# Kernel optimization log

Hardware: AMD Instinct MI355X
Metric: run time of the kernel (lower is better)

The kernel has to match this reference:

```python
import jax, jax.numpy as jnp
import numpy as np

DIM = 1024
H = 16
DH = 64
ORDER = 3
TOPK = 64
SCALE = DH ** (-0.5)


def setup_inputs() -> dict:
    key = jax.random.key(0)
    k0, k1, k2 = jax.random.split(key, 3)
    B, N = 2, 2048
    inner = H * DH
    x = jax.random.normal(k0, (B, N, DIM), jnp.float32)
    Wqkv = jax.random.normal(k1, (DIM, 3 * inner), jnp.float32) * (DIM ** -0.5)
    bqkv = jnp.zeros((3 * inner,), jnp.float32)
    Wout = jax.random.normal(k2, (inner, DIM), jnp.float32) * (inner ** -0.5)
    bout = jnp.zeros((DIM,), jnp.float32)
    # init_as_standard_attention for sigmoid act: zero_val=-5, one_val=+5 on row 1
    alphas_raw = jnp.full((ORDER + 1, H), -5.0, jnp.float32).at[1].set(5.0)
    return {"x": x, "Wqkv": Wqkv, "bqkv": bqkv, "Wout": Wout, "bout": bout,
            "alphas_raw": alphas_raw}


def reference(x, Wqkv, bqkv, Wout, bout, alphas_raw):
    B, N, _ = x.shape
    qkv = x @ Wqkv + bqkv                          # [B,N,3*inner]
    q, k, v = jnp.split(qkv, 3, axis=-1)
    to_heads = lambda t: t.reshape(B, N, H, DH).transpose(0, 2, 1, 3)  # [B,H,N,DH]
    q, k, v = to_heads(q), to_heads(k), to_heads(v)
    scores = jnp.einsum('bhnd,bhmd->bhnm', q, k) * SCALE
    # top-k sparsification: drop entries strictly below the k-th largest per row
    if TOPK and TOPK < N:
        kth = jax.lax.top_k(scores, TOPK)[0][..., -1:]  # [B,H,N,1]
        scores = jnp.where(scores < kth, -jnp.inf, scores)
    attn = jax.nn.softmax(scores, axis=-1)          # [B,H,N,N]
    # polynomial graph filter in fp32 (monomial basis, learn_zero_order=False)
    alphas = jax.nn.sigmoid(alphas_raw)             # [ORDER+1, H]
    v_curr = v
    res = jnp.zeros_like(v)
    for i in range(1, ORDER + 1):
        v_curr = jnp.einsum('bhnm,bhmd->bhnd', attn, v_curr)
        res = res + alphas[i][None, :, None, None] * v_curr
    out = res.transpose(0, 2, 1, 3).reshape(B, N, H * DH)
    return out @ Wout + bout
```

## Files before the change

kernel.cpp:

```cpp
#include <hip/hip_runtime.h>
#include <cstdint>
#include <cstddef>

#define HHEADS 16
#define DHEAD  64
#define NSEQ   2048
#define NBATCH 2
#define NDIM   1024
#define TOPKN  64
#define CAP    68
#define NROWS  (NBATCH*HHEADS*NSEQ)

__global__ __launch_bounds__(256) void qkv_gemm(
    const float* __restrict__ x, const float* __restrict__ W,
    const float* __restrict__ bias,
    float* __restrict__ qout, float* __restrict__ kout, float* __restrict__ vout)
{
    __shared__ float As[16][128];
    __shared__ float Bs[16][128];
    const int tid = threadIdx.x;
    const int rowBase = blockIdx.y * 128;
    const int colBase = blockIdx.x * 128;
    const int tx = tid & 15, ty = tid >> 4;
    const int arow = tid & 127, akq = tid >> 7;
    const int bkk = tid >> 5,  bc4 = tid & 31;

    float acc[8][8] = {};
    float4 a0 = *reinterpret_cast<const float4*>(&x[(size_t)(rowBase + arow) * NDIM + akq * 4]);
    float4 a1 = *reinterpret_cast<const float4*>(&x[(size_t)(rowBase + arow) * NDIM + (akq + 2) * 4]);
    float4 b0 = *reinterpret_cast<const float4*>(&W[(size_t)bkk * 3072 + colBase + bc4 * 4]);
    float4 b1 = *reinterpret_cast<const float4*>(&W[(size_t)(bkk + 8) * 3072 + colBase + bc4 * 4]);

    for (int k0 = 0; k0 < NDIM; k0 += 16) {
        __syncthreads();
        As[akq * 4 + 0][arow] = a0.x; As[akq * 4 + 1][arow] = a0.y;
        As[akq * 4 + 2][arow] = a0.z; As[akq * 4 + 3][arow] = a0.w;
        As[(akq + 2) * 4 + 0][arow] = a1.x; As[(akq + 2) * 4 + 1][arow] = a1.y;
        As[(akq + 2) * 4 + 2][arow] = a1.z; As[(akq + 2) * 4 + 3][arow] = a1.w;
        *reinterpret_cast<float4*>(&Bs[bkk][bc4 * 4])     = b0;
        *reinterpret_cast<float4*>(&Bs[bkk + 8][bc4 * 4]) = b1;
        __syncthreads();
        if (k0 + 16 < NDIM) {
            a0 = *reinterpret_cast<const float4*>(&x[(size_t)(rowBase + arow) * NDIM + k0 + 16 + akq * 4]);
            a1 = *reinterpret_cast<const float4*>(&x[(size_t)(rowBase + arow) * NDIM + k0 + 16 + (akq + 2) * 4]);
            b0 = *reinterpret_cast<const float4*>(&W[(size_t)(k0 + 16 + bkk) * 3072 + colBase + bc4 * 4]);
            b1 = *reinterpret_cast<const float4*>(&W[(size_t)(k0 + 16 + bkk + 8) * 3072 + colBase + bc4 * 4]);
        }
#pragma unroll
        for (int kk = 0; kk < 16; kk++) {
            float4 alo = *reinterpret_cast<const float4*>(&As[kk][ty * 4]);
            float4 ahi = *reinterpret_cast<const float4*>(&As[kk][64 + ty * 4]);
            float4 blo = *reinterpret_cast<const float4*>(&Bs[kk][tx * 4]);
            float4 bhi = *reinterpret_cast<const float4*>(&Bs[kk][64 + tx * 4]);
            float ar[8] = {alo.x, alo.y, alo.z, alo.w, ahi.x, ahi.y, ahi.z, ahi.w};
            float br[8] = {blo.x, blo.y, blo.z, blo.w, bhi.x, bhi.y, bhi.z, bhi.w};
#pragma unroll
            for (int i = 0; i < 8; i++)
#pragma unroll
                for (int j = 0; j < 8; j++) acc[i][j] += ar[i] * br[j];
        }
    }

    const int which = colBase >> 10;
    float* dst = which == 0 ? qout : (which == 1 ? kout : vout);
#pragma unroll
    for (int jh = 0; jh < 2; jh++) {
        const int colh = colBase + jh * 64 + tx * 4;
        const int h = (colh & 1023) >> 6;
        const int d0 = colh & 63;
        float4 bb = *reinterpret_cast<const float4*>(&bias[colh]);
#pragma unroll
        for (int ih = 0; ih < 2; ih++)
#pragma unroll
            for (int i = 0; i < 4; i++) {
                int r = rowBase + ih * 64 + ty * 4 + i;
                int b = r >> 11, n = r & 2047;
                size_t o = ((size_t)((b << 4) + h) * NSEQ + n) * DHEAD + d0;
                float4 st;
                st.x = acc[ih * 4 + i][jh * 4 + 0] + bb.x;
                st.y = acc[ih * 4 + i][jh * 4 + 1] + bb.y;
                st.z = acc[ih * 4 + i][jh * 4 + 2] + bb.z;
                st.w = acc[ih * 4 + i][jh * 4 + 3] + bb.w;
                *reinterpret_cast<float4*>(&dst[o]) = st;
            }
    }
}

__device__ __forceinline__ uint32_t f2key(float f) {
    uint32_t u = __float_as_uint(f);
    return (u & 0x80000000u) ? ~u : (u | 0x80000000u);
}
__device__ __forceinline__ float key2f(uint32_t k) {
    uint32_t u = (k & 0x80000000u) ? (k & 0x7FFFFFFFu) : ~k;
    return __uint_as_float(u);
}

__device__ __forceinline__ void topk_emit(
    uint32_t (&k)[32], float m, int row, int lane,
    int* __restrict__ tki, float* __restrict__ tkp, int* __restrict__ tkc)
{
    uint32_t lo = 0u, hi = 0xFFFFFFFFu;
    while (lo < hi) {
        uint32_t mid = (uint32_t)(((uint64_t)lo + (uint64_t)hi + 1ull) >> 1);
        int c = 0;
#pragma unroll
        for (int t = 0; t < 32; t++)
            c += (int)__popcll(__ballot(k[t] >= mid));
        if (c >= TOPKN) { lo = mid; if (c == TOPKN) { hi = mid; } }
        else hi = mid - 1;
    }
    const uint32_t thr = lo;

    uint32_t keep = 0;
    float sum = 0.f;
#pragma unroll
    for (int t = 0; t < 32; t++) {
        bool kp = (k[t] >= thr);
        float e = kp ? __expf(key2f(k[t]) - m) : 0.f;
        k[t] = __float_as_uint(e);
        sum += e;
        keep |= kp ? (1u << t) : 0u;
    }
#pragma unroll
    for (int off = 32; off >= 1; off >>= 1) sum += __shfl_xor(sum, off);
    const float rs = 1.f / sum;

    int base = 0;
    const unsigned long long below = (1ull << lane) - 1ull;
#pragma unroll
    for (int t = 0; t < 32; t++) {
        bool kp = (keep >> t) & 1u;
        unsigned long long mask = __ballot(kp);
        if (kp) {
            int pos = base + (int)__popcll(mask & below);
            if (pos < CAP) {
                tki[(size_t)row * CAP + pos] = ((t >> 2) << 8) + (lane << 2) + (t & 3);
                tkp[(size_t)row * CAP + pos] = __uint_as_float(k[t]) * rs;
            }
        }
        base += (int)__popcll(mask);
    }
    if (lane == 0) tkc[row] = base < CAP ? base : CAP;
}

__device__ __forceinline__ void gload_lds16(const void* g, void* l) {
    __builtin_amdgcn_global_load_lds(
        (const __attribute__((address_space(1))) unsigned int*)g,
        (__attribute__((address_space(3))) unsigned int*)l,
        16, 0, 0);
}

__global__ __launch_bounds__(256) void scores_gemm(
    const float* __restrict__ qg, const float* __restrict__ kg,
    uint32_t* __restrict__ keyg, int n0, int Nc)
{
    __shared__ float Qs[64][128];
    __shared__ float Kb[64][64];
    const int tid = threadIdx.x;
    const int bh = blockIdx.z;
    const int rowBase = n0 + blockIdx.y * 128;
    const int colBase = blockIdx.x * 64;
    const int tx = tid & 15, ty = tid >> 4;

    {
        const int arow = tid & 127, g = tid >> 7;
        const float* qrow = &qg[((size_t)bh * NSEQ + rowBase + arow) * DHEAD];
#pragma unroll
        for (int j = 0; j < 8; j++) {
            int f = g * 8 + j;
            float4 v = *reinterpret_cast<const float4*>(qrow + f * 4);
            Qs[f * 4 + 0][arow] = v.x; Qs[f * 4 + 1][arow] = v.y;
            Qs[f * 4 + 2][arow] = v.z; Qs[f * 4 + 3][arow] = v.w;
        }
    }
    {
        const int j = tid & 63, g = tid >> 6;
        const float* krow = &kg[((size_t)bh * NSEQ + colBase + j) * DHEAD];
#pragma unroll
        for (int i = 0; i < 4; i++) {
            int f = g * 4 + i;
            float4 v = *reinterpret_cast<const float4*>(krow + f * 4);
            Kb[f * 4 + 0][j] = v.x; Kb[f * 4 + 1][j] = v.y;
            Kb[f * 4 + 2][j] = v.z; Kb[f * 4 + 3][j] = v.w;
        }
    }
    __syncthreads();

    float acc[8][4] = {};
#pragma unroll
    for (int kk = 0; kk < 64; kk++) {
        float4 q0 = *reinterpret_cast<const float4*>(&Qs[kk][ty * 8]);
        float4 q1 = *reinterpret_cast<const float4*>(&Qs[kk][ty * 8 + 4]);
        float4 kv = *reinterpret_cast<const float4*>(&Kb[kk][tx * 4]);
        float qr[8] = {q0.x, q0.y, q0.z, q0.w, q1.x, q1.y, q1.z, q1.w};
        float kr[4] = {kv.x, kv.y, kv.z, kv.w};
#pragma unroll
        for (int r = 0; r < 8; r++)
#pragma unroll
            for (int c = 0; c < 4; c++) acc[r][c] += qr[r] * kr[c];
    }

    const size_t rloc0 = (size_t)bh * Nc + (blockIdx.y * 128 + ty * 8);
#pragma unroll
    for (int r = 0; r < 8; r++) {
        uint4 kv4;
        kv4.x = f2key(acc[r][0] * 0.125f);
        kv4.y = f2key(acc[r][1] * 0.125f);
        kv4.z = f2key(acc[r][2] * 0.125f);
        kv4.w = f2key(acc[r][3] * 0.125f);
        *reinterpret_cast<uint4*>(&keyg[(rloc0 + r) * 2048 + colBase + tx * 4]) = kv4;
    }
}

__global__ __launch_bounds__(256) void topk_kernel(
    const uint32_t* __restrict__ keyg,
    int* __restrict__ tki, float* __restrict__ tkp, int* __restrict__ tkc,
    int n0, int lgNc)
{
    const int rloc = blockIdx.x * 4 + (threadIdx.x >> 6);
    const int lane = threadIdx.x & 63;
    const int bh = rloc >> lgNc;
    const int n  = n0 + (rloc & ((1 << lgNc) - 1));
    const int row = (bh << 11) + n;
    const uint4* src = reinterpret_cast<const uint4*>(keyg + (size_t)rloc * 2048);

    uint32_t k[32];
#pragma unroll
    for (int p = 0; p < 8; p++) {
        uint4 c4 = src[p * 64 + lane];
        k[p * 4 + 0] = c4.x; k[p * 4 + 1] = c4.y;
        k[p * 4 + 2] = c4.z; k[p * 4 + 3] = c4.w;
    }
    uint32_t km = 0;
#pragma unroll
    for (int t = 0; t < 32; t++) km = k[t] > km ? k[t] : km;
#pragma unroll
    for (int off = 32; off >= 1; off >>= 1) {
        uint32_t o = __shfl_xor(km, off);
        km = o > km ? o : km;
    }
    topk_emit(k, key2f(km), row, lane, tki, tkp, tkc);
}

__global__ __launch_bounds__(256) void scores_topk(
    const float* __restrict__ qg, const float* __restrict__ kg,
    int* __restrict__ tki, float* __restrict__ tkp, int* __restrict__ tkc)
{
    __shared__ float4   Ks[2][2048];
    __shared__ float    qs[8][64];
    __shared__ uint32_t keyk[8][2048];
    const int bh = blockIdx.y;
    const int wave = threadIdx.x >> 6, lane = threadIdx.x & 63;
    const size_t kbase = (size_t)bh * NSEQ * DHEAD;

    if (threadIdx.x < 128) {
        int r = threadIdx.x >> 4, c4 = threadIdx.x & 15;
        *reinterpret_cast<float4*>(&qs[r][c4 << 2]) =
            *reinterpret_cast<const float4*>(
                &qg[((size_t)bh * NSEQ + blockIdx.x * 8 + r) * DHEAD + (c4 << 2)]);
    }

    const int jw  = wave * 4 + (lane >> 4);
    const int swz = lane & 15;
    auto stage = [&](int T, int buf) {
#pragma unroll
        for (int rep = 0; rep < 8; rep++) {
            int j = rep * 16 + jw;
            int c = swz ^ (j & 7);
            gload_lds16(&kg[kbase + (size_t)(T * 128 + j) * DHEAD + (c << 2)],
                        (char*)&Ks[buf][0] + (rep * 4096 + wave * 1024));
        }
    };

    stage(0, 0);
    __syncthreads();

    const int rA = wave * 2, rB = rA + 1;
    float mA = -3.4e38f, mB = -3.4e38f;

    for (int KT = 0; KT < 16; KT++) {
        const int cur = KT & 1;
        if (KT < 15) stage(KT + 1, cur ^ 1);

        float sA0 = 0.f, sA1 = 0.f, sB0 = 0.f, sB1 = 0.f;
#pragma unroll
        for (int c = 0; c < 16; c++) {
            float4 qa = *reinterpret_cast<const float4*>(&qs[rA][c << 2]);
            float4 qb = *reinterpret_cast<const float4*>(&qs[rB][c << 2]);
            int j0 = lane, j1 = 64 + lane;
            float4 kv0 = Ks[cur][(j0 << 4) + (c ^ (j0 & 7))];
            float4 kv1 = Ks[cur][(j1 << 4) + (c ^ (j1 & 7))];
            sA0 += qa.x * kv0.x + qa.y * kv0.y + qa.z * kv0.z + qa.w * kv0.w;
            sA1 += qa.x * kv1.x + qa.y * kv1.y + qa.z * kv1.z + qa.w * kv1.w;
            sB0 += qb.x * kv0.x + qb.y * kv0.y + qb.z * kv0.z + qb.w * kv0.w;
            sB1 += qb.x * kv1.x + qb.y * kv1.y + qb.z * kv1.z + qb.w * kv1.w;
        }
        sA0 *= 0.125f; sA1 *= 0.125f; sB0 *= 0.125f; sB1 *= 0.125f;
        mA = fmaxf(mA, fmaxf(sA0, sA1));
        mB = fmaxf(mB, fmaxf(sB0, sB1));
        keyk[rA][KT * 128 + lane]      = f2key(sA0);
        keyk[rA][KT * 128 + 64 + lane] = f2key(sA1);
        keyk[rB][KT * 128 + lane]      = f2key(sB0);
        keyk[rB][KT * 128 + 64 + lane] = f2key(sB1);
        __syncthreads();
    }

#pragma unroll
    for (int off = 32; off >= 1; off >>= 1) {
        mA = fmaxf(mA, __shfl_xor(mA, off));
        mB = fmaxf(mB, __shfl_xor(mB, off));
    }

    const int rowA = bh * NSEQ + blockIdx.x * 8 + wave * 2;
    {
        const uint4* src = reinterpret_cast<const uint4*>(&keyk[rA][0]);
        uint32_t k[32];
#pragma unroll
        for (int p = 0; p < 8; p++) {
            uint4 c4 = src[p * 64 + lane];
            k[p * 4 + 0] = c4.x; k[p * 4 + 1] = c4.y;
            k[p * 4 + 2] = c4.z; k[p * 4 + 3] = c4.w;
        }
        topk_emit(k, mA, rowA, lane, tki, tkp, tkc);
    }
    {
        const uint4* src = reinterpret_cast<const uint4*>(&keyk[rB][0]);
        uint32_t k[32];
#pragma unroll
        for (int p = 0; p < 8; p++) {
            uint4 c4 = src[p * 64 + lane];
            k[p * 4 + 0] = c4.x; k[p * 4 + 1] = c4.y;
            k[p * 4 + 2] = c4.z; k[p * 4 + 3] = c4.w;
        }
        topk_emit(k, mB, rowA + 1, lane, tki, tkp, tkc);
    }
}

__global__ __launch_bounds__(256) void prop(
    const float* __restrict__ vin, float* __restrict__ vout,
    float* __restrict__ res, const float* __restrict__ araw,
    const int* __restrict__ tki, const float* __restrict__ tkp,
    const int* __restrict__ tkc, int iter)
{
    const int row = blockIdx.x * 4 + (threadIdx.x >> 6);
    const int lane = threadIdx.x & 63;
    const int bh = row >> 11;
    const int h = bh & 15;
    const int cnt = tkc[row];
    const int* idx = tki + (size_t)row * CAP;
    const float* pr = tkp + (size_t)row * CAP;
    const float* vb = vin + (size_t)bh * NSEQ * DHEAD;

    float a0 = 0.f, a1 = 0.f, a2 = 0.f, a3 = 0.f;
    int j = 0;
    for (; j + 4 <= cnt; j += 4) {
        int i0 = idx[j], i1 = idx[j + 1], i2 = idx[j + 2], i3 = idx[j + 3];
        float p0 = pr[j], p1 = pr[j + 1], p2 = pr[j + 2], p3 = pr[j + 3];
        a0 += p0 * vb[(size_t)i0 * DHEAD + lane];
        a1 += p1 * vb[(size_t)i1 * DHEAD + lane];
        a2 += p2 * vb[(size_t)i2 * DHEAD + lane];
        a3 += p3 * vb[(size_t)i3 * DHEAD + lane];
    }
    for (; j < cnt; j++) a0 += pr[j] * vb[(size_t)idx[j] * DHEAD + lane];
    float acc = (a0 + a1) + (a2 + a3);

    vout[(size_t)row * DHEAD + lane] = acc;

    float ar = araw[iter * HHEADS + h];
    float alpha = 1.f / (1.f + __expf(-ar));
    const int b = row >> 15, n = row & 2047;
    size_t ro = ((size_t)(b * NSEQ + n)) * 1024 + h * DHEAD + lane;
    if (iter == 1) res[ro] = alpha * acc;
    else           res[ro] += alpha * acc;
}

__global__ __launch_bounds__(256) void out_gemm(
    const float* __restrict__ A, const float* __restrict__ W,
    const float* __restrict__ bias, float* __restrict__ out)
{
    __shared__ float As[16][64];
    __shared__ float Bs[16][64];
    const int tid = threadIdx.x;
    const int rowBase = blockIdx.y * 64;
    const int colBase = blockIdx.x * 64;
    const int tx = tid & 15, ty = tid >> 4;
    const int aRow = tid >> 2, aCol = (tid & 3) << 2;
    const int bRow = tid >> 4, bCol = (tid & 15) << 2;

    float acc[4][4] = {};
    for (int k0 = 0; k0 < 1024; k0 += 16) {
        float4 av = *reinterpret_cast<const float4*>(&A[(size_t)(rowBase + aRow) * 1024 + k0 + aCol]);
        float4 bv = *reinterpret_cast<const float4*>(&W[(size_t)(k0 + bRow) * 1024 + colBase + bCol]);
        __syncthreads();
        As[aCol + 0][aRow] = av.x; As[aCol + 1][aRow] = av.y;
        As[aCol + 2][aRow] = av.z; As[aCol + 3][aRow] = av.w;
        *reinterpret_cast<float4*>(&Bs[bRow][bCol]) = bv;
        __syncthreads();
#pragma unroll
        for (int kk = 0; kk < 16; kk++) {
            float4 a4 = *reinterpret_cast<const float4*>(&As[kk][ty << 2]);
            float4 b4 = *reinterpret_cast<const float4*>(&Bs[kk][tx << 2]);
            float ar[4] = {a4.x, a4.y, a4.z, a4.w};
            float br[4] = {b4.x, b4.y, b4.z, b4.w};
#pragma unroll
            for (int i = 0; i < 4; i++)
#pragma unroll
                for (int j = 0; j < 4; j++) acc[i][j] += ar[i] * br[j];
        }
    }
    float4 bb = *reinterpret_cast<const float4*>(&bias[colBase + (tx << 2)]);
#pragma unroll
    for (int i = 0; i < 4; i++) {
        int r = rowBase + (ty << 2) + i;
        float4 st;
        st.x = acc[i][0] + bb.x; st.y = acc[i][1] + bb.y;
        st.z = acc[i][2] + bb.z; st.w = acc[i][3] + bb.w;
        *reinterpret_cast<float4*>(&out[(size_t)r * 1024 + colBase + (tx << 2)]) = st;
    }
}

extern "C" void kernel_launch(void* const* d_in, const int* in_sizes, int n_in,
                              void* d_out, int out_size, void* d_ws, size_t ws_size,
                              hipStream_t stream)
{
    const float* x    = (const float*)d_in[0];
    const float* Wqkv = (const float*)d_in[1];
    const float* bqkv = (const float*)d_in[2];
    const float* Wout = (const float*)d_in[3];
    const float* bout = (const float*)d_in[4];
    const float* araw = (const float*)d_in[5];
    float* out = (float*)d_out;

    const size_t SEG = (size_t)1 << 22;
    float* ws = (float*)d_ws;
    float* q   = ws;
    float* k   = q + SEG;
    float* v   = k + SEG;
    int*   tki = (int*)(v + SEG);
    float* tkp = (float*)(tki + (size_t)NROWS * CAP);
    int*   tkc = (int*)(tkp + (size_t)NROWS * CAP);
    uint32_t* keyg = (uint32_t*)(tkc + NROWS);
    float* vA  = (float*)keyg;
    float* res = q;

    const size_t keyg_off = (size_t)((char*)keyg - (char*)d_ws);
    const size_t leftover = ws_size > keyg_off ? ws_size - keyg_off : 0;

    int Nc = NSEQ;
    while (Nc >= 128 && (((size_t)Nc) << 18) > leftover) Nc >>= 1;

    qkv_gemm<<<dim3(24, 32), 256, 0, stream>>>(x, Wqkv, bqkv, q, k, v);

    if (Nc >= 128) {
        int lgNc = __builtin_ctz((unsigned)Nc);
        for (int n0 = 0; n0 < NSEQ; n0 += Nc) {
            scores_gemm<<<dim3(32, Nc / 128, 32), 256, 0, stream>>>(q, k, keyg, n0, Nc);
            topk_kernel<<<dim3(32 * Nc / 4), 256, 0, stream>>>(keyg, tki, tkp, tkc, n0, lgNc);
        }
    } else {
        scores_topk<<<dim3(256, 32), 256, 0, stream>>>(q, k, tki, tkp, tkc);
    }

    prop<<<dim3(NROWS / 4), 256, 0, stream>>>(v,  vA, res, araw, tki, tkp, tkc, 1);
    prop<<<dim3(NROWS / 4), 256, 0, stream>>>(vA, v,  res, araw, tki, tkp, tkc, 2);
    prop<<<dim3(NROWS / 4), 256, 0, stream>>>(v,  vA, res, araw, tki, tkp, tkc, 3);
    out_gemm<<<dim3(16, 64), 256, 0, stream>>>(res, Wout, bout, out);
}
```

Baseline: 1.212 ms.

## Deepen GEMM K-tiles, enlarge out_gemm tile, vectorize prop index loads

The QKV GEMM now stages 32-deep K slices instead of 16, which halves the number of barrier rounds. The output GEMM moves to 128x64 tiles with 8x4 per-thread accumulators, 32-deep K slices and register prefetch of the next slice. The prop kernel reads its top-k indices and weights as int4/float4 vectors. These target sync overhead, operand reuse and load instruction count, in exchange for more shared memory and registers, which may lower occupancy. The int4 loads assume 16-byte alignment, which holds because CAP is 68.

Result: slower. 1.264 ms (+4.3%).

```diff
diff --git a/kernel.cpp b/kernel.cpp
--- a/kernel.cpp
+++ b/kernel.cpp
@@ -16,38 +16,48 @@
     const float* __restrict__ bias,
     float* __restrict__ qout, float* __restrict__ kout, float* __restrict__ vout)
 {
-    __shared__ float As[16][128];
-    __shared__ float Bs[16][128];
+    __shared__ float As[32][128];
+    __shared__ float Bs[32][128];
     const int tid = threadIdx.x;
     const int rowBase = blockIdx.y * 128;
     const int colBase = blockIdx.x * 128;
     const int tx = tid & 15, ty = tid >> 4;
-    const int arow = tid & 127, akq = tid >> 7;
+    const int arow = tid & 127, ag = (tid >> 7) << 4;
     const int bkk = tid >> 5,  bc4 = tid & 31;
 
     float acc[8][8] = {};
-    float4 a0 = *reinterpret_cast<const float4*>(&x[(size_t)(rowBase + arow) * NDIM + akq * 4]);
-    float4 a1 = *reinterpret_cast<const float4*>(&x[(size_t)(rowBase + arow) * NDIM + (akq + 2) * 4]);
-    float4 b0 = *reinterpret_cast<const float4*>(&W[(size_t)bkk * 3072 + colBase + bc4 * 4]);
-    float4 b1 = *reinterpret_cast<const float4*>(&W[(size_t)(bkk + 8) * 3072 + colBase + bc4 * 4]);
-
-    for (int k0 = 0; k0 < NDIM; k0 += 16) {
+    float4 ap[4], bp[4];
+    const float* xrow = &x[(size_t)(rowBase + arow) * NDIM];
+#pragma unroll
+    for (int j = 0; j < 4; j++)
+        ap[j] = *reinterpret_cast<const float4*>(xrow + ag + j * 4);
+#pragma unroll
+    for (int i = 0; i < 4; i++)
+        bp[i] = *reinterpret_cast<const float4*>(&W[(size_t)(bkk + 8 * i) * 3072 + colBase + bc4 * 4]);
+
+    for (int k0 = 0; k0 < NDIM; k0 += 32) {
         __syncthreads();
-        As[akq * 4 + 0][arow] = a0.x; As[akq * 4 + 1][arow] = a0.y;
-        As[akq * 4 + 2][arow] = a0.z; As[akq * 4 + 3][arow] = a0.w;
-        As[(akq + 2) * 4 + 0][arow] = a1.x; As[(akq + 2) * 4 + 1][arow] = a1.y;
-        As[(akq + 2) * 4 + 2][arow] = a1.z; As[(akq + 2) * 4 + 3][arow] = a1.w;
-        *reinterpret_cast<float4*>(&Bs[bkk][bc4 * 4])     = b0;
-        *reinterpret_cast<float4*>(&Bs[bkk + 8][bc4 * 4]) = b1;
+#pragma unroll
+        for (int j = 0; j < 4; j++) {
+            As[ag + j * 4 + 0][arow] = ap[j].x;
+            As[ag + j * 4 + 1][arow] = ap[j].y;
+            As[ag + j * 4 + 2][arow] = ap[j].z;
+            As[ag + j * 4 + 3][arow] = ap[j].w;
+        }
+#pragma unroll
+        for (int i = 0; i < 4; i++)
+            *reinterpret_cast<float4*>(&Bs[bkk + 8 * i][bc4 * 4]) = bp[i];
         __syncthreads();
-        if (k0 + 16 < NDIM) {
-            a0 = *reinterpret_cast<const float4*>(&x[(size_t)(rowBase + arow) * NDIM + k0 + 16 + akq * 4]);
-            a1 = *reinterpret_cast<const float4*>(&x[(size_t)(rowBase + arow) * NDIM + k0 + 16 + (akq + 2) * 4]);
-            b0 = *reinterpret_cast<const float4*>(&W[(size_t)(k0 + 16 + bkk) * 3072 + colBase + bc4 * 4]);
-            b1 = *reinterpret_cast<const float4*>(&W[(size_t)(k0 + 16 + bkk + 8) * 3072 + colBase + bc4 * 4]);
-        }
-#pragma unroll
-        for (int kk = 0; kk < 16; kk++) {
+        if (k0 + 32 < NDIM) {
+#pragma unroll
+            for (int j = 0; j < 4; j++)
+                ap[j] = *reinterpret_cast<const float4*>(xrow + k0 + 32 + ag + j * 4);
+#pragma unroll
+            for (int i = 0; i < 4; i++)
+                bp[i] = *reinterpret_cast<const float4*>(&W[(size_t)(k0 + 32 + bkk + 8 * i) * 3072 + colBase + bc4 * 4]);
+        }
+#pragma unroll
+        for (int kk = 0; kk < 32; kk++) {
             float4 alo = *reinterpret_cast<const float4*>(&As[kk][ty * 4]);
             float4 ahi = *reinterpret_cast<const float4*>(&As[kk][64 + ty * 4]);
             float4 blo = *reinterpret_cast<const float4*>(&Bs[kk][tx * 4]);
@@ -354,12 +364,12 @@
     float a0 = 0.f, a1 = 0.f, a2 = 0.f, a3 = 0.f;
     int j = 0;
     for (; j + 4 <= cnt; j += 4) {
-        int i0 = idx[j], i1 = idx[j + 1], i2 = idx[j + 2], i3 = idx[j + 3];
-        float p0 = pr[j], p1 = pr[j + 1], p2 = pr[j + 2], p3 = pr[j + 3];
-        a0 += p0 * vb[(size_t)i0 * DHEAD + lane];
-        a1 += p1 * vb[(size_t)i1 * DHEAD + lane];
-        a2 += p2 * vb[(size_t)i2 * DHEAD + lane];
-        a3 += p3 * vb[(size_t)i3 * DHEAD + lane];
+        int4   i4 = *reinterpret_cast<const int4*>(&idx[j]);
+        float4 p4 = *reinterpret_cast<const float4*>(&pr[j]);
+        a0 += p4.x * vb[(size_t)i4.x * DHEAD + lane];
+        a1 += p4.y * vb[(size_t)i4.y * DHEAD + lane];
+        a2 += p4.z * vb[(size_t)i4.z * DHEAD + lane];
+        a3 += p4.w * vb[(size_t)i4.w * DHEAD + lane];
     }
     for (; j < cnt; j++) a0 += pr[j] * vb[(size_t)idx[j] * DHEAD + lane];
     float acc = (a0 + a1) + (a2 + a3);
@@ -378,44 +388,68 @@
     const float* __restrict__ A, const float* __restrict__ W,
     const float* __restrict__ bias, float* __restrict__ out)
 {
-    __shared__ float As[16][64];
-    __shared__ float Bs[16][64];
+    __shared__ float As[32][128];
+    __shared__ float Bs[32][64];
     const int tid = threadIdx.x;
-    const int rowBase = blockIdx.y * 64;
+    const int rowBase = blockIdx.y * 128;
     const int colBase = blockIdx.x * 64;
     const int tx = tid & 15, ty = tid >> 4;
-    const int aRow = tid >> 2, aCol = (tid & 3) << 2;
-    const int bRow = tid >> 4, bCol = (tid & 15) << 2;
-
-    float acc[4][4] = {};
-    for (int k0 = 0; k0 < 1024; k0 += 16) {
-        float4 av = *reinterpret_cast<const float4*>(&A[(size_t)(rowBase + aRow) * 1024 + k0 + aCol]);
-        float4 bv = *reinterpret_cast<const float4*>(&W[(size_t)(k0 + bRow) * 1024 + colBase + bCol]);
+    const int arow = tid & 127, ag = (tid >> 7) << 4;
+    const int bkk = tid >> 4,  bc4 = tid & 15;
+
+    float acc[8][4] = {};
+    float4 ap[4], bp[2];
+    const float* Arow = &A[(size_t)(rowBase + arow) * 1024];
+#pragma unroll
+    for (int j = 0; j < 4; j++)
+        ap[j] = *reinterpret_cast<const float4*>(Arow + ag + j * 4);
+#pragma unroll
+    for (int i = 0; i < 2; i++)
+        bp[i] = *reinterpret_cast<const float4*>(&W[(size_t)(bkk + 16 * i) * 1024 + colBase + bc4 * 4]);
+
+    for (int k0 = 0; k0 < 1024; k0 += 32) {
         __syncthreads();
-        As[aCol + 0][aRow] = av.x; As[aCol + 1][aRow] = av.y;
-        As[aCol + 2][aRow] = av.z; As[aCol + 3][aRow] = av.w;
-        *reinterpret_cast<float4*>(&Bs[bRow][bCol]) = bv;
+#pragma unroll
+        for (int j = 0; j < 4; j++) {
+            As[ag + j * 4 + 0][arow] = ap[j].x;
+            As[ag + j * 4 + 1][arow] = ap[j].y;
+            As[ag + j * 4 + 2][arow] = ap[j].z;
+            As[ag + j * 4 + 3][arow] = ap[j].w;
+        }
+#pragma unroll
+        for (int i = 0; i < 2; i++)
+            *reinterpret_cast<float4*>(&Bs[bkk + 16 * i][bc4 * 4]) = bp[i];
         __syncthreads();
-#pragma unroll
-        for (int kk = 0; kk < 16; kk++) {
-            float4 a4 = *reinterpret_cast<const float4*>(&As[kk][ty << 2]);
-            float4 b4 = *reinterpret_cast<const float4*>(&Bs[kk][tx << 2]);
-            float ar[4] = {a4.x, a4.y, a4.z, a4.w};
-            float br[4] = {b4.x, b4.y, b4.z, b4.w};
-#pragma unroll
-            for (int i = 0; i < 4; i++)
-#pragma unroll
-                for (int j = 0; j < 4; j++) acc[i][j] += ar[i] * br[j];
-        }
-    }
-    float4 bb = *reinterpret_cast<const float4*>(&bias[colBase + (tx << 2)]);
-#pragma unroll
-    for (int i = 0; i < 4; i++) {
-        int r = rowBase + (ty << 2) + i;
+        if (k0 + 32 < 1024) {
+#pragma unroll
+            for (int j = 0; j < 4; j++)
+                ap[j] = *reinterpret_cast<const float4*>(Arow + k0 + 32 + ag + j * 4);
+#pragma unroll
+            for (int i = 0; i < 2; i++)
+                bp[i] = *reinterpret_cast<const float4*>(&W[(size_t)(k0 + 32 + bkk + 16 * i) * 1024 + colBase + bc4 * 4]);
+        }
+#pragma unroll
+        for (int kk = 0; kk < 32; kk++) {
+            float4 a0 = *reinterpret_cast<const float4*>(&As[kk][ty * 8]);
+            float4 a1 = *reinterpret_cast<const float4*>(&As[kk][ty * 8 + 4]);
+            float4 bv = *reinterpret_cast<const float4*>(&Bs[kk][tx * 4]);
+            float qr[8] = {a0.x, a0.y, a0.z, a0.w, a1.x, a1.y, a1.z, a1.w};
+            float br[4] = {bv.x, bv.y, bv.z, bv.w};
+#pragma unroll
+            for (int r = 0; r < 8; r++)
+#pragma unroll
+                for (int c = 0; c < 4; c++) acc[r][c] += qr[r] * br[c];
+        }
+    }
+
+    float4 bb = *reinterpret_cast<const float4*>(&bias[colBase + tx * 4]);
+#pragma unroll
+    for (int r = 0; r < 8; r++) {
+        int row = rowBase + ty * 8 + r;
         float4 st;
-        st.x = acc[i][0] + bb.x; st.y = acc[i][1] + bb.y;
-        st.z = acc[i][2] + bb.z; st.w = acc[i][3] + bb.w;
-        *reinterpret_cast<float4*>(&out[(size_t)r * 1024 + colBase + (tx << 2)]) = st;
+        st.x = acc[r][0] + bb.x; st.y = acc[r][1] + bb.y;
+        st.z = acc[r][2] + bb.z; st.w = acc[r][3] + bb.w;
+        *reinterpret_cast<float4*>(&out[(size_t)row * 1024 + colBase + tx * 4]) = st;
     }
 }
 
@@ -464,5 +498,5 @@
     prop<<<dim3(NROWS / 4), 256, 0, stream>>>(v,  vA, res, araw, tki, tkp, tkc, 1);
     prop<<<dim3(NROWS / 4), 256, 0, stream>>>(vA, v,  res, araw, tki, tkp, tkc, 2);
     prop<<<dim3(NROWS / 4), 256, 0, stream>>>(v,  vA, res, araw, tki, tkp, tkc, 3);
-    out_gemm<<<dim3(16, 64), 256, 0, stream>>>(res, Wout, bout, out);
-}
+    out_gemm<<<dim3(16, 32), 256, 0, stream>>>(res, Wout, bout, out);
+}
```
